# Optimization experiments

Hardware: AMD Instinct MI355X
Metric: run time of the kernel (lower is better)

The kernel has to match this reference:

```python
import jax, jax.numpy as jnp
import numpy as np


def _selective_scan(u, delta, A, Bm, Cm, Dskip, delta_bias):
    # u, delta: (B, K*D, L); A: (K*D, N); Bm, Cm: (B, K, N, L); Dskip, delta_bias: (K*D,)
    Bsz, KD, L = u.shape
    K = Bm.shape[1]
    D = KD // K
    N = A.shape[1]
    dt = jax.nn.softplus(delta + delta_bias[None, :, None])          # (B,KD,L)
    u4 = u.reshape(Bsz, K, D, L)
    dt4 = dt.reshape(Bsz, K, D, L)
    A4 = A.reshape(K, D, N)
    # discretization: dA = exp(dt*A), dBu = dt * B * u
    dA = jnp.exp(dt4[..., None] * A4[None, :, :, None, :])            # (B,K,D,L,N)
    Bt = jnp.transpose(Bm, (0, 1, 3, 2))                               # (B,K,L,N)
    dBu = dt4[..., None] * u4[..., None] * Bt[:, :, None, :, :]        # (B,K,D,L,N)
    dA_l = jnp.moveaxis(dA, 3, 0)                                      # (L,B,K,D,N)
    dBu_l = jnp.moveaxis(dBu, 3, 0)

    def step(h, ab):
        a, b = ab
        h = a * h + b
        return h, h

    h0 = jnp.zeros(dA_l.shape[1:], dA.dtype)
    _, hs = jax.lax.scan(step, h0, (dA_l, dBu_l))                      # (L,B,K,D,N)
    C_l = jnp.moveaxis(Cm, 3, 0)                                       # (L,B,K,N)
    y = jnp.einsum('lbkdn,lbkn->lbkd', hs, C_l)                        # (L,B,K,D)
    y = jnp.moveaxis(y, 0, 3).reshape(Bsz, KD, L)
    return y + u * Dskip[None, :, None]


def setup_inputs() -> dict:
    key = jax.random.key(0)
    ks = jax.random.split(key, 8)
    B, H, W, C = 2, 64, 64, 96
    Di, N, K = 192, 16, 4
    R = 6  # ceil(96/16)
    x = jax.random.normal(ks[0], (B, H, W, C), jnp.float32)
    in_proj_w = jax.random.normal(ks[1], (2 * Di, C), jnp.float32) * (C ** -0.5)
    conv_w = jax.random.normal(ks[2], (Di, 1, 3, 3), jnp.float32) * 0.2
    conv_b = jax.random.normal(ks[3], (Di,), jnp.float32) * 0.02
    x_proj_weight = jax.random.normal(ks[4], (K, R + 2 * N, Di), jnp.float32) * (Di ** -0.5)
    dt_projs_weight = jax.random.uniform(ks[5], (K, Di, R), jnp.float32, -(R ** -0.5), R ** -0.5)
    dt = jnp.exp(jax.random.uniform(ks[6], (K, Di), jnp.float32) * (np.log(0.1) - np.log(0.001)) + np.log(0.001))
    dt = jnp.clip(dt, 1e-4)
    dt_projs_bias = dt + jnp.log(-jnp.expm1(-dt))                      # inverse softplus
    A_logs = jnp.log(jnp.tile(jnp.arange(1, N + 1, dtype=jnp.float32), (K * Di, 1)))
    Ds = jnp.ones((K * Di,), jnp.float32)
    out_norm_w = jnp.ones((Di,), jnp.float32)
    out_norm_b = jnp.zeros((Di,), jnp.float32)
    out_proj_w = jax.random.normal(ks[7], (C, Di), jnp.float32) * (Di ** -0.5)
    return dict(x=x, in_proj_w=in_proj_w, conv_w=conv_w, conv_b=conv_b,
                x_proj_weight=x_proj_weight, dt_projs_weight=dt_projs_weight,
                dt_projs_bias=dt_projs_bias, A_logs=A_logs, Ds=Ds,
                out_norm_w=out_norm_w, out_norm_b=out_norm_b, out_proj_w=out_proj_w)


def reference(x, in_proj_w, conv_w, conv_b, x_proj_weight, dt_projs_weight,
              dt_projs_bias, A_logs, Ds, out_norm_w, out_norm_b, out_proj_w):
    Bsz, H, W, C = x.shape
    Di = conv_w.shape[0]
    K = x_proj_weight.shape[0]
    R = dt_projs_weight.shape[2]
    N = A_logs.shape[1]
    L = H * W
    # in_proj (bias=False) and split into x, z
    xz = x @ in_proj_w.T                                               # (B,H,W,2*Di)
    xi, z = jnp.split(xz, 2, axis=-1)
    # depthwise conv2d + SiLU (channel-first)
    xc = jnp.transpose(xi, (0, 3, 1, 2))                               # (B,Di,H,W)
    xc = jax.lax.conv_general_dilated(xc, conv_w, (1, 1), 'SAME',
                                      feature_group_count=Di) + conv_b[None, :, None, None]
    xc = jax.nn.silu(xc)
    # cross-scan: 4 directions (row-major, col-major, and their reverses)
    x0 = xc.reshape(Bsz, Di, L)
    x1 = jnp.transpose(xc, (0, 1, 3, 2)).reshape(Bsz, Di, L)
    xs = jnp.stack([x0, x1, x0[..., ::-1], x1[..., ::-1]], axis=1)      # (B,K,Di,L)
    # per-direction projections
    x_dbl = jnp.einsum('bkdl,kcd->bkcl', xs, x_proj_weight)            # (B,K,R+2N,L)
    dts, Bs, Cs = jnp.split(x_dbl, [R, R + N], axis=2)
    dts = jnp.einsum('bkrl,kdr->bkdl', dts, dt_projs_weight)           # (B,K,Di,L)
    A = -jnp.exp(A_logs)                                               # (K*Di,N)
    ys = _selective_scan(xs.reshape(Bsz, K * Di, L), dts.reshape(Bsz, K * Di, L),
                         A, Bs, Cs, Ds, dt_projs_bias.reshape(-1))
    ys = ys.reshape(Bsz, K, Di, L)
    # cross-merge
    y = ys[:, 0] + ys[:, 2, :, ::-1]
    yt = ys[:, 1] + ys[:, 3, :, ::-1]                                  # col-major ordering
    y = y + jnp.transpose(yt.reshape(Bsz, Di, W, H), (0, 1, 3, 2)).reshape(Bsz, Di, L)
    y = jnp.transpose(y.reshape(Bsz, Di, H, W), (0, 2, 3, 1))          # (B,H,W,Di)
    # out_norm: LayerNorm over channel
    mu = jnp.mean(y, axis=-1, keepdims=True)
    var = jnp.mean((y - mu) ** 2, axis=-1, keepdims=True)
    y = (y - mu) * jax.lax.rsqrt(var + 1e-5) * out_norm_w + out_norm_b
    # gate and out_proj (bias=False)
    y = y * jax.nn.silu(z)
    return y @ out_proj_w.T
```

## Files before the change

### kernel.cpp

```cpp
#include <hip/hip_runtime.h>
#include <hip/hip_fp16.h>
#include <math.h>


static constexpr int Bsz = 2;
static constexpr int Lc  = 4096;
static constexpr int Cc  = 96;
static constexpr int Dd  = 192;
static constexpr int Kk  = 4;
static constexpr int NC  = 32;

__device__ __forceinline__ float bu(unsigned short v) {
    return __uint_as_float((unsigned int)v << 16);
}
__device__ __forceinline__ unsigned short f2b(float f) {
    unsigned int u = __float_as_uint(f);
    return (unsigned short)((u + 0x7fffu + ((u >> 16) & 1u)) >> 16);
}

template<int CTRL>
__device__ __forceinline__ float dppadd(float x) {
    return x + __int_as_float(__builtin_amdgcn_update_dpp(
        0, __float_as_int(x), CTRL, 0xf, 0xf, true));
}
__device__ __forceinline__ float red16(float x) {
    x = dppadd<0xB1>(x);
    x = dppadd<0x4E>(x);
    x = dppadd<0x124>(x);
    x = dppadd<0x128>(x);
    return x;
}

__global__ __launch_bounds__(256) void k0_detect(const unsigned short* __restrict__ x,
                                                 int* __restrict__ flag)
{
    __shared__ int s[256];
    int cnt = 0;
    for (int i = threadIdx.x; i < 4096; i += 256) {
        int e = (x[i] >> 7) & 0xFF;
        cnt += (e >= 118 && e <= 131) ? 1 : 0;
    }
    s[threadIdx.x] = cnt;
    __syncthreads();
    for (int st = 128; st > 0; st >>= 1) {
        if (threadIdx.x < st) s[threadIdx.x] += s[threadIdx.x + st];
        __syncthreads();
    }
    if (threadIdx.x == 0) flag[0] = (s[0] >= 3072) ? 1 : 0;
}

struct Cv {
    const void* src[11];
    int off[11];
    int n[11];
};
__global__ __launch_bounds__(256) void k0b_convert(Cv cv, const int* __restrict__ flag,
                                                   float* __restrict__ dstbase)
{
    int bf = flag[0];
    int t = blockIdx.y;
    int i = blockIdx.x * 256 + threadIdx.x;
    if (i >= cv.n[t]) return;
    float v;
    if (bf) v = bu(((const unsigned short*)cv.src[t])[i]);
    else    v = ((const float*)cv.src[t])[i];
    dstbase[cv.off[t] + i] = v;
}

__global__ __launch_bounds__(256) void k3w_prep(const float* __restrict__ xpwf,
                                                float* __restrict__ Wg)
{
    int idx = blockIdx.x * 256 + threadIdx.x;
    if (idx >= 4 * 192 * 40) return;
    int cp = idx % 40;
    int d  = (idx / 40) % 192;
    int k  = idx / 7680;
    Wg[idx] = (cp < 38) ? xpwf[(size_t)(k * 38 + cp) * 192 + d] : 0.f;
}

__global__ __launch_bounds__(256) void k1_inproj(const void* __restrict__ xraw,
                                                 const int* __restrict__ flag,
                                                 const float* __restrict__ wf,
                                                 float* __restrict__ xi, __half* __restrict__ zs)
{
    __shared__ float xT[32 * 97];
    __shared__ float wT[96 * 97];
    const int bf = flag[0];
    int tile = blockIdx.x >> 2, jq = blockIdx.x & 3;
    int b = tile >> 7;
    int l0 = (tile & 127) << 5;
    int j0 = jq * 96;
    for (int e = threadIdx.x; e < 32 * 96; e += 256) {
        int i = e / 96, c = e % 96;
        size_t idx = (size_t)(b * Lc + l0 + i) * Cc + c;
        xT[i * 97 + c] = bf ? bu(((const unsigned short*)xraw)[idx])
                            : ((const float*)xraw)[idx];
    }
    for (int e = threadIdx.x; e < 96 * 96; e += 256) {
        int j = e / 96, c = e % 96;
        wT[j * 97 + c] = wf[(size_t)(j0 + j) * Cc + c];
    }
    __syncthreads();
    int jj = threadIdx.x & 31, ll = threadIdx.x >> 5;
    float acc[4][3];
#pragma unroll
    for (int i = 0; i < 4; i++)
#pragma unroll
        for (int m = 0; m < 3; m++) acc[i][m] = 0.f;
    for (int c = 0; c < 96; ++c) {
        float xv[4], wv[3];
#pragma unroll
        for (int i = 0; i < 4; i++) xv[i] = xT[(ll * 4 + i) * 97 + c];
#pragma unroll
        for (int m = 0; m < 3; m++) wv[m] = wT[(jj + 32 * m) * 97 + c];
#pragma unroll
        for (int i = 0; i < 4; i++)
#pragma unroll
            for (int m = 0; m < 3; m++) acc[i][m] += xv[i] * wv[m];
    }
#pragma unroll
    for (int i = 0; i < 4; i++) {
        int l = l0 + ll * 4 + i;
#pragma unroll
        for (int m = 0; m < 3; m++) {
            int j = j0 + jj + 32 * m;
            float v = acc[i][m];
            if (j < Dd) xi[(size_t)(b * Lc + l) * Dd + j] = v;
            else        zs[(size_t)(b * Lc + l) * Dd + (j - Dd)] = __float2half(v / (1.f + __expf(-v)));
        }
    }
}

__global__ __launch_bounds__(256) void k2a_transpose(const float* __restrict__ xi,
                                                     float* __restrict__ xiT)
{
    __shared__ float t[64 * 65];
    int bid = blockIdx.x;
    int lq = bid & 63, dq = (bid >> 6) % 3, b = bid / 192;
    int l0 = lq * 64, d0 = dq * 64;
    for (int e = threadIdx.x; e < 4096; e += 256) {
        int i = e >> 6, j = e & 63;
        t[i * 65 + j] = xi[(size_t)(b * Lc + l0 + i) * Dd + d0 + j];
    }
    __syncthreads();
    for (int e = threadIdx.x; e < 4096; e += 256) {
        int j = e >> 6, i = e & 63;
        xiT[(size_t)(b * Dd + d0 + j) * Lc + l0 + i] = t[i * 65 + j];
    }
}

__global__ __launch_bounds__(256) void k2b_conv(const float* __restrict__ xiT,
                                                const float* __restrict__ cwf,
                                                const float* __restrict__ cbf,
                                                float* __restrict__ xc,
                                                float* __restrict__ uT)
{
    __shared__ float inl[34 * 66];
    __shared__ float outl[32 * 65];
    int bid = blockIdx.x;
    int half = bid & 1;
    int d = (bid >> 1) % Dd;
    int b = bid / (2 * Dd);
    int h0 = half * 32;
    const float* src = xiT + (size_t)(b * Dd + d) * Lc;
    for (int r = threadIdx.x; r < 34; r += 256) {
        inl[r * 66 + 0] = 0.f;
        inl[r * 66 + 65] = 0.f;
    }
    for (int e = threadIdx.x; e < 34 * 64; e += 256) {
        int row = e >> 6, w = e & 63;
        int h = h0 - 1 + row;
        inl[row * 66 + 1 + w] = (h >= 0 && h < 64) ? src[h * 64 + w] : 0.f;
    }
    __syncthreads();
    float wgt[9];
#pragma unroll
    for (int t = 0; t < 9; t++) wgt[t] = cwf[d * 9 + t];
    float bias = cbf[d];
    int hs = threadIdx.x >> 6, w = threadIdx.x & 63;
    float* dstrow = xc + (size_t)(b * Dd + d) * Lc;
#pragma unroll
    for (int it = 0; it < 8; ++it) {
        int hh = it * 4 + hs;
        float acc = bias;
#pragma unroll
        for (int dy = 0; dy < 3; ++dy) {
            const float* rp = &inl[(hh + dy) * 66 + w];
#pragma unroll
            for (int dx = 0; dx < 3; ++dx)
                acc += rp[dx] * wgt[dy * 3 + dx];
        }
        float s = acc / (1.f + __expf(-acc));
        dstrow[(h0 + hh) * 64 + w] = s;
        outl[hh * 65 + w] = s;
    }
    __syncthreads();
    float* udst = uT + (size_t)(b * Dd + d) * Lc;
    for (int e = threadIdx.x; e < 2048; e += 256) {
        int w2 = e >> 5, hh2 = e & 31;
        udst[w2 * 64 + h0 + hh2] = outl[hh2 * 65 + w2];
    }
}

__global__ __launch_bounds__(256) void k3_proj(const float* __restrict__ xc,
                                               const float* __restrict__ uT,
                                               const float* __restrict__ Wg,
                                               const float* __restrict__ dtwf,
                                               const float* __restrict__ dtbf,
                                               __half* __restrict__ dtH,
                                               float* __restrict__ BsT, float* __restrict__ CsT)
{
    __shared__ float rawdt[6][64];
    int bid = blockIdx.x;
    int pt = bid & 63, k = (bid >> 6) & 3, b = bid >> 8;
    int s0 = pt * 64;
    int pi = threadIdx.x & 63;
    int q  = __builtin_amdgcn_readfirstlane(threadIdx.x >> 6);

    const float* xb = ((k & 1) ? uT : xc) + (size_t)b * Dd * Lc + s0 + pi;
    const float* wk = Wg + (size_t)k * 192 * 40 + q * 10;

    float acc[10];
#pragma unroll
    for (int j = 0; j < 10; ++j) acc[j] = 0.f;

    for (int d = 0; d < 192; ++d) {
        float xv = xb[(size_t)d * Lc];
        const float* wrow = wk + d * 40;
#pragma unroll
        for (int j = 0; j < 10; ++j) acc[j] += wrow[j] * xv;
    }

    if (q == 0) {
#pragma unroll
        for (int j = 0; j < 6; ++j) rawdt[j][pi] = acc[j];
    }
    size_t bk16 = (size_t)(b * Kk + k) * 16;
#pragma unroll
    for (int j = 0; j < 10; ++j) {
        int cp = q * 10 + j;
        if (cp >= 6 && cp < 22)
            BsT[(bk16 + (cp - 6)) * Lc + s0 + pi] = acc[j];
        else if (cp >= 22 && cp < 38)
            CsT[(bk16 + (cp - 22)) * Lc + s0 + pi] = acc[j];
    }
    __syncthreads();

    float raws[6];
#pragma unroll
    for (int r = 0; r < 6; ++r) raws[r] = rawdt[r][pi];
    const float* dtw = dtwf + (size_t)(k * 192 + q * 48) * 6;
    const float* dtb = dtbf + k * 192 + q * 48;
    __half* dto = dtH + ((size_t)(b * Kk + k) * Dd + q * 48) * Lc + s0 + pi;
    for (int dd = 0; dd < 48; ++dd) {
        float s = dtb[dd];
#pragma unroll
        for (int r = 0; r < 6; ++r) s += raws[r] * dtw[dd * 6 + r];
        float sp = fmaxf(s, 0.f) + log1pf(__expf(-fabsf(s)));
        dto[(size_t)dd * Lc] = __float2half(sp);
    }
}

template<int REV, int PASS3>
__device__ __forceinline__ void scan_run(const float* __restrict__ ubase,
                                         const __half* __restrict__ dbase,
                                         const float* __restrict__ Bbase,
                                         const float* __restrict__ Cbase,
                                         float* uL, float* bL, float* cL, __half* dL,
                                         int dl, int n, int c,
                                         float An, float Dsv,
                                         float* __restrict__ P, float* __restrict__ S,
                                         size_t pidx, __half* __restrict__ yrow)
{
    const int t0 = c * 128;
    const int tg = REV ? (Lc - 128 - t0) : t0;

    {
        float4 ru0 = *reinterpret_cast<const float4*>(ubase + tg + n * 4);
        float4 ru1 = *reinterpret_cast<const float4*>(ubase + tg + 64 + n * 4);
        float4 rb0 = *reinterpret_cast<const float4*>(Bbase + tg + n * 4);
        float4 rb1 = *reinterpret_cast<const float4*>(Bbase + tg + 64 + n * 4);
        uint4  rd  = *reinterpret_cast<const uint4*>(dbase + tg + n * 8);
        *reinterpret_cast<float4*>(uL + dl * 132 + n * 4) = ru0;
        *reinterpret_cast<float4*>(uL + dl * 132 + 64 + n * 4) = ru1;
        *reinterpret_cast<float4*>(bL + dl * 132 + n * 4) = rb0;
        *reinterpret_cast<float4*>(bL + dl * 132 + 64 + n * 4) = rb1;
        *reinterpret_cast<uint4*>(dL + dl * 136 + n * 8) = rd;
        if (PASS3) {
            float4 rc0 = *reinterpret_cast<const float4*>(Cbase + tg + n * 4);
            float4 rc1 = *reinterpret_cast<const float4*>(Cbase + tg + 64 + n * 4);
            *reinterpret_cast<float4*>(cL + dl * 132 + n * 4) = rc0;
            *reinterpret_cast<float4*>(cL + dl * 132 + 64 + n * 4) = rc1;
        }
    }
    __syncthreads();

    float h = PASS3 ? P[pidx] : 0.f;
    float sdt = 0.f, ystash = 0.f;

#pragma unroll 4
    for (int qi = 0; qi < 32; ++qi) {
        const int col4 = REV ? (124 - qi * 4) : (qi * 4);
        float4 uq = *reinterpret_cast<const float4*>(uL + dl * 132 + col4);
        float4 bq = *reinterpret_cast<const float4*>(bL + n * 132 + col4);
        float4 cq{};
        if (PASS3) cq = *reinterpret_cast<const float4*>(cL + n * 132 + col4);
        uint2 dq = *reinterpret_cast<const uint2*>(dL + dl * 136 + col4);
        const __half2* dh2 = reinterpret_cast<const __half2*>(&dq);
#pragma unroll
        for (int j = 0; j < 4; ++j) {
            const int e = REV ? (3 - j) : j;
            float dtv = (e & 1) ? __high2float(dh2[e >> 1]) : __low2float(dh2[e >> 1]);
            float uv = reinterpret_cast<const float*>(&uq)[e];
            float bv = reinterpret_cast<const float*>(&bq)[e];
            float a = __expf(dtv * An);
            if (!PASS3) sdt += dtv;
            h = a * h + (dtv * uv) * bv;
            if (PASS3) {
                float cv = reinterpret_cast<const float*>(&cq)[e];
                float yv = red16(h * cv);
                const int i15 = (qi & 3) * 4 + j;
                if (i15 == n) ystash = yv + uv * Dsv;
                if (i15 == 15) {
                    int tb = t0 + (qi >> 2) * 16 + n;
                    int aw = REV ? (Lc - 1 - tb) : tb;
                    yrow[aw] = __float2half(ystash);
                }
            }
        }
    }

    if (!PASS3) {
        P[pidx] = __expf(An * sdt);
        S[pidx] = h;
    }
}

template<int PASS3>
__global__ __launch_bounds__(256) void kscan(const __half* __restrict__ dtH,
                                             const float* __restrict__ xc,
                                             const float* __restrict__ uT,
                                             const float* __restrict__ BsT,
                                             const float* __restrict__ CsT,
                                             const float* __restrict__ alogf,
                                             const float* __restrict__ dsf,
                                             float* __restrict__ P,
                                             float* __restrict__ S,
                                             __half* __restrict__ ysH)
{
    __shared__ float uL[16 * 132];
    __shared__ float bL[16 * 132];
    __shared__ float cL[PASS3 ? 16 * 132 : 4];
    __shared__ __half dL[16 * 136];

    int c  = blockIdx.x & 31;
    int t1 = blockIdx.x >> 5;
    int dg = t1 % 12;
    int kk = (t1 / 12) & 3;
    int b  = t1 / 48;
    int n  = threadIdx.x & 15, dl = threadIdx.x >> 4;
    int d  = dg * 16 + dl;

    const float* ubz = ((kk & 1) ? uT : xc) + (size_t)b * Dd * Lc;
    const float*  ubase = ubz + (size_t)d * Lc;
    const __half* dbase = dtH + ((size_t)((b * Kk + kk) * Dd + d)) * Lc;
    const float*  Bbase = BsT + ((size_t)((b * Kk + kk) * 16 + dl)) * Lc;
    const float*  Cbase = CsT + ((size_t)((b * Kk + kk) * 16 + dl)) * Lc;

    float An  = -__expf(alogf[(kk * Dd + d) * 16 + n]);
    float Dsv = PASS3 ? dsf[kk * Dd + d] : 0.f;
    size_t pidx = (((size_t)(b * Kk + kk) * Dd + d) * NC + c) * 16 + n;
    __half* yrow = PASS3 ? ysH + ((size_t)(kk * Bsz + b) * Dd + d) * Lc : nullptr;

    if (kk >= 2)
        scan_run<1, PASS3>(ubase, dbase, Bbase, Cbase, uL, bL, cL, dL,
                           dl, n, c, An, Dsv, P, S, pidx, yrow);
    else
        scan_run<0, PASS3>(ubase, dbase, Bbase, Cbase, uL, bL, cL, dL,
                           dl, n, c, An, Dsv, P, S, pidx, yrow);
}

__global__ __launch_bounds__(256) void k6_pass2(float* __restrict__ P, const float* __restrict__ S)
{
    int g = blockIdx.x * 256 + threadIdx.x;
    int n = g & 15;
    int chain = g >> 4;
    size_t base = (size_t)chain * NC * 16 + n;
    float h = 0.f;
    for (int c = 0; c < NC; ++c) {
        size_t id = base + (size_t)c * 16;
        float p = P[id], s = S[id];
        P[id] = h;
        h = p * h + s;
    }
}

__global__ __launch_bounds__(256) void k8t(const __half* __restrict__ ysH,
                                           __half* __restrict__ ysT)
{
    __shared__ float t[64 * 65];
    int bid = blockIdx.x;
    int d = bid % Dd, b = bid / Dd;
    const __half* y1 = ysH + ((size_t)(1 * Bsz + b) * Dd + d) * Lc;
    const __half* y3 = ysH + ((size_t)(3 * Bsz + b) * Dd + d) * Lc;
    __half* dst = ysT + ((size_t)b * Dd + d) * Lc;
    for (int e = threadIdx.x; e < 4096; e += 256)
        t[(e >> 6) * 65 + (e & 63)] = __half2float(y1[e]) + __half2float(y3[e]);
    __syncthreads();
    for (int e = threadIdx.x; e < 4096; e += 256)
        dst[e] = __float2half(t[(e & 63) * 65 + (e >> 6)]);
}

__global__ __launch_bounds__(256) void k8_norm(const __half* __restrict__ ysH,
                                               const __half* __restrict__ ysT,
                                               const __half* __restrict__ zsH,
                                               const float* __restrict__ nwf,
                                               const float* __restrict__ nbf,
                                               __half* __restrict__ gH)
{
    __shared__ float yt[192 * 33];
    __shared__ float ps1[8 * 32], ps2[8 * 32];
    __shared__ float mu[32], rs[32];
    int bid = blockIdx.x;
    int pt = bid & 127, b = bid >> 7;
    int p0 = pt * 32;
    for (int e = threadIdx.x; e < 192 * 32; e += 256) {
        int d = e >> 5, p = e & 31;
        size_t r0 = ((size_t)(0 * Bsz + b) * Dd + d) * Lc + p0 + p;
        size_t r2 = ((size_t)(2 * Bsz + b) * Dd + d) * Lc + p0 + p;
        size_t rt = ((size_t)b * Dd + d) * Lc + p0 + p;
        yt[d * 33 + p] = __half2float(ysH[r0]) + __half2float(ysH[r2]) + __half2float(ysT[rt]);
    }
    __syncthreads();
    {
        int p = threadIdx.x & 31, q = threadIdx.x >> 5;
        float s1 = 0.f, s2 = 0.f;
        for (int dd = 0; dd < 24; ++dd) {
            float v = yt[(q * 24 + dd) * 33 + p];
            s1 += v; s2 += v * v;
        }
        ps1[q * 32 + p] = s1; ps2[q * 32 + p] = s2;
    }
    __syncthreads();
    if (threadIdx.x < 32) {
        int p = threadIdx.x;
        float s1 = 0.f, s2 = 0.f;
        for (int q = 0; q < 8; ++q) { s1 += ps1[q * 32 + p]; s2 += ps2[q * 32 + p]; }
        float m = s1 * (1.f / 192.f);
        float var = s2 * (1.f / 192.f) - m * m;
        mu[p] = m; rs[p] = rsqrtf(var + 1e-5f);
    }
    __syncthreads();
    for (int i = threadIdx.x; i < 32 * 192; i += 256) {
        int p = i / 192, d = i - p * 192;
        float v = (yt[d * 33 + p] - mu[p]) * rs[p] * nwf[d] + nbf[d];
        size_t addr = ((size_t)b * Lc + p0 + p) * Dd + d;
        float zv = __half2float(zsH[addr]);
        gH[addr] = __float2half(v * zv);
    }
}

__global__ __launch_bounds__(256) void k10_outproj(const __half* __restrict__ gH,
                                                   const float* __restrict__ wof,
                                                   const int* __restrict__ flag,
                                                   void* __restrict__ outv)
{
    __shared__ float wT[192 * 100];
    const int bf = flag[0];
    for (int e = threadIdx.x; e < 96 * 192; e += 256) {
        int cI = e / 192, dI = e - cI * 192;
        wT[dI * 100 + cI] = wof[e];
    }
    __syncthreads();
    int r0 = blockIdx.x * 32;
    int r = threadIdx.x >> 3, cg = threadIdx.x & 7;
    const __half* grow = gH + (size_t)(r0 + r) * Dd;
    float acc[12];
#pragma unroll
    for (int i = 0; i < 12; ++i) acc[i] = 0.f;
    for (int d0 = 0; d0 < 192; d0 += 8) {
        __half2 g2[4];
        *reinterpret_cast<uint4*>(g2) = *reinterpret_cast<const uint4*>(grow + d0);
#pragma unroll
        for (int j = 0; j < 8; ++j) {
            float gf = (j & 1) ? __high2float(g2[j >> 1]) : __low2float(g2[j >> 1]);
            const float* wrow = &wT[(d0 + j) * 100 + cg * 12];
            float4 w0 = *reinterpret_cast<const float4*>(wrow);
            float4 w1 = *reinterpret_cast<const float4*>(wrow + 4);
            float4 w2 = *reinterpret_cast<const float4*>(wrow + 8);
            acc[0] += gf * w0.x; acc[1] += gf * w0.y; acc[2]  += gf * w0.z; acc[3]  += gf * w0.w;
            acc[4] += gf * w1.x; acc[5] += gf * w1.y; acc[6]  += gf * w1.z; acc[7]  += gf * w1.w;
            acc[8] += gf * w2.x; acc[9] += gf * w2.y; acc[10] += gf * w2.z; acc[11] += gf * w2.w;
        }
    }
    size_t obase = (size_t)(r0 + r) * Cc + cg * 12;
    if (bf) {
        unsigned short* o = (unsigned short*)outv;
#pragma unroll
        for (int cc = 0; cc < 12; ++cc) o[obase + cc] = f2b(acc[cc]);
    } else {
        float* o = (float*)outv;
#pragma unroll
        for (int cc = 0; cc < 12; ++cc) o[obase + cc] = acc[cc];
    }
}

extern "C" void kernel_launch(void* const* d_in, const int* in_sizes, int n_in,
                              void* d_out, int out_size, void* d_ws, size_t ws_size,
                              hipStream_t stream)
{
    (void)out_size; (void)ws_size;
    float* ws = (float*)d_ws;
    int* flag = (int*)ws;

    int off[12]; int tot = 64;
    off[0] = 0;
    for (int i = 1; i < 12; ++i) {
        off[i] = tot;
        int n = (i < n_in) ? in_sizes[i] : 0;
        tot += (n + 63) & ~63;
    }
    float* winf = ws + off[1];
    float* cwf  = ws + off[2];
    float* cbf  = ws + off[3];
    float* xpwf = ws + off[4];
    float* dtwf = ws + off[5];
    float* dtbf = ws + off[6];
    float* alogf= ws + off[7];
    float* dsf  = ws + off[8];
    float* nwf  = ws + off[9];
    float* nbf  = ws + off[10];
    float* wof  = ws + off[11];

    const size_t BASE = 131072;
    __half* dtH = (__half*)(ws + BASE);
    float*  xc  = ws + BASE + 3145728;
    float*  uT  = ws + BASE + 4718592;
    float*  BsT = ws + BASE + 6291456;
    float*  CsT = ws + BASE + 6815744;
    float*  P   = ws + BASE + 7340032;
    float*  S   = ws + BASE + 8126464;
    __half* zsH = (__half*)(ws + BASE + 8912896);
    float*  xi  = ws + BASE + 9699328;
    float*  xiT = ws + BASE + 9699328 + 1572864;
    __half* ysH = (__half*)(ws + BASE + 9699328);
    __half* ysT = (__half*)P;
    __half* gH  = (__half*)S;
    float*  Wg  = ws + BASE + 12845056;

    Cv cv;
    for (int i = 0; i < 11; ++i) {
        int t = i + 1;
        cv.src[i] = (t < n_in) ? d_in[t] : d_in[0];
        cv.off[i] = off[t];
        cv.n[i]   = (t < n_in) ? in_sizes[t] : 0;
    }

    k0_detect   <<<dim3(1),    dim3(256), 0, stream>>>((const unsigned short*)d_in[0], flag);
    k0b_convert <<<dim3(144, 11), dim3(256), 0, stream>>>(cv, flag, ws);
    k3w_prep    <<<dim3(120),  dim3(256), 0, stream>>>(xpwf, Wg);
    k1_inproj   <<<dim3(1024), dim3(256), 0, stream>>>(d_in[0], flag, winf, xi, zsH);
    k2a_transpose<<<dim3(384), dim3(256), 0, stream>>>(xi, xiT);
    k2b_conv    <<<dim3(768),  dim3(256), 0, stream>>>(xiT, cwf, cbf, xc, uT);
    k3_proj     <<<dim3(512),  dim3(256), 0, stream>>>(xc, uT, Wg, dtwf, dtbf, dtH, BsT, CsT);
    kscan<0>    <<<dim3(3072), dim3(256), 0, stream>>>(dtH, xc, uT, BsT, CsT, alogf, dsf, P, S, ysH);
    k6_pass2    <<<dim3(96),   dim3(256), 0, stream>>>(P, S);
    kscan<1>    <<<dim3(3072), dim3(256), 0, stream>>>(dtH, xc, uT, BsT, CsT, alogf, dsf, P, S, ysH);
    k8t         <<<dim3(384),  dim3(256), 0, stream>>>(ysH, ysT);
    k8_norm     <<<dim3(256),  dim3(256), 0, stream>>>(ysH, ysT, zsH, nwf, nbf, gH);
    k10_outproj <<<dim3(256),  dim3(256), 0, stream>>>(gH, wof, flag, d_out);
}
```

Before: 200.8 us.

## Fuse transpose into in-proj, fold weight prep and D-skip into other kernels

The in-projection now writes its x half directly in channel-major layout and z as a transposed half-precision gate, which removes the separate transpose kernel. The x_proj weight repack is merged into the input conversion kernel as an extra grid row. The D-skip term leaves the scan kernel; the norm kernel adds it once, using the summed D across the four directions applied to the conv output. The pass-2 kernel now runs 64-thread blocks with an unrolled loop. Together these cut two launches and one full intermediate round trip, at the cost of weights being read from global memory inside the in-proj inner loop instead of from LDS.

```diff
diff --git a/kernel.cpp b/kernel.cpp
--- a/kernel.cpp
+++ b/kernel.cpp
@@ -50,9 +50,9 @@
 }
 
 struct Cv {
-    const void* src[11];
-    int off[11];
-    int n[11];
+    const void* src[12];
+    int off[12];
+    int n[12];
 };
 __global__ __launch_bounds__(256) void k0b_convert(Cv cv, const int* __restrict__ flag,
                                                    float* __restrict__ dstbase)
@@ -61,91 +61,72 @@
     int t = blockIdx.y;
     int i = blockIdx.x * 256 + threadIdx.x;
     if (i >= cv.n[t]) return;
+    if (t == 11) {
+        int cp = i % 40;
+        int d  = (i / 40) % 192;
+        int k  = i / 7680;
+        float v = 0.f;
+        if (cp < 38) {
+            size_t si = (size_t)(k * 38 + cp) * 192 + d;
+            v = bf ? bu(((const unsigned short*)cv.src[11])[si])
+                   : ((const float*)cv.src[11])[si];
+        }
+        dstbase[cv.off[11] + i] = v;
+        return;
+    }
     float v;
     if (bf) v = bu(((const unsigned short*)cv.src[t])[i]);
     else    v = ((const float*)cv.src[t])[i];
     dstbase[cv.off[t] + i] = v;
 }
 
-__global__ __launch_bounds__(256) void k3w_prep(const float* __restrict__ xpwf,
-                                                float* __restrict__ Wg)
-{
-    int idx = blockIdx.x * 256 + threadIdx.x;
-    if (idx >= 4 * 192 * 40) return;
-    int cp = idx % 40;
-    int d  = (idx / 40) % 192;
-    int k  = idx / 7680;
-    Wg[idx] = (cp < 38) ? xpwf[(size_t)(k * 38 + cp) * 192 + d] : 0.f;
-}
-
 __global__ __launch_bounds__(256) void k1_inproj(const void* __restrict__ xraw,
                                                  const int* __restrict__ flag,
                                                  const float* __restrict__ wf,
-                                                 float* __restrict__ xi, __half* __restrict__ zs)
-{
-    __shared__ float xT[32 * 97];
-    __shared__ float wT[96 * 97];
+                                                 float* __restrict__ xiT, __half* __restrict__ zT)
+{
+    __shared__ float xT[64 * 97];
     const int bf = flag[0];
-    int tile = blockIdx.x >> 2, jq = blockIdx.x & 3;
-    int b = tile >> 7;
-    int l0 = (tile & 127) << 5;
-    int j0 = jq * 96;
-    for (int e = threadIdx.x; e < 32 * 96; e += 256) {
+    int lt = blockIdx.x & 127;
+    int jq = blockIdx.x >> 7;
+    int row0 = lt * 64;
+    for (int e = threadIdx.x; e < 64 * 96; e += 256) {
         int i = e / 96, c = e % 96;
-        size_t idx = (size_t)(b * Lc + l0 + i) * Cc + c;
+        size_t idx = (size_t)(row0 + i) * Cc + c;
         xT[i * 97 + c] = bf ? bu(((const unsigned short*)xraw)[idx])
                             : ((const float*)xraw)[idx];
     }
-    for (int e = threadIdx.x; e < 96 * 96; e += 256) {
-        int j = e / 96, c = e % 96;
-        wT[j * 97 + c] = wf[(size_t)(j0 + j) * Cc + c];
-    }
-    __syncthreads();
-    int jj = threadIdx.x & 31, ll = threadIdx.x >> 5;
-    float acc[4][3];
-#pragma unroll
-    for (int i = 0; i < 4; i++)
-#pragma unroll
-        for (int m = 0; m < 3; m++) acc[i][m] = 0.f;
-    for (int c = 0; c < 96; ++c) {
-        float xv[4], wv[3];
-#pragma unroll
-        for (int i = 0; i < 4; i++) xv[i] = xT[(ll * 4 + i) * 97 + c];
-#pragma unroll
-        for (int m = 0; m < 3; m++) wv[m] = wT[(jj + 32 * m) * 97 + c];
-#pragma unroll
-        for (int i = 0; i < 4; i++)
-#pragma unroll
-            for (int m = 0; m < 3; m++) acc[i][m] += xv[i] * wv[m];
-    }
-#pragma unroll
-    for (int i = 0; i < 4; i++) {
-        int l = l0 + ll * 4 + i;
-#pragma unroll
-        for (int m = 0; m < 3; m++) {
-            int j = j0 + jj + 32 * m;
-            float v = acc[i][m];
-            if (j < Dd) xi[(size_t)(b * Lc + l) * Dd + j] = v;
-            else        zs[(size_t)(b * Lc + l) * Dd + (j - Dd)] = __float2half(v / (1.f + __expf(-v)));
-        }
-    }
-}
-
-__global__ __launch_bounds__(256) void k2a_transpose(const float* __restrict__ xi,
-                                                     float* __restrict__ xiT)
-{
-    __shared__ float t[64 * 65];
-    int bid = blockIdx.x;
-    int lq = bid & 63, dq = (bid >> 6) % 3, b = bid / 192;
-    int l0 = lq * 64, d0 = dq * 64;
-    for (int e = threadIdx.x; e < 4096; e += 256) {
-        int i = e >> 6, j = e & 63;
-        t[i * 65 + j] = xi[(size_t)(b * Lc + l0 + i) * Dd + d0 + j];
-    }
-    __syncthreads();
-    for (int e = threadIdx.x; e < 4096; e += 256) {
-        int j = e >> 6, i = e & 63;
-        xiT[(size_t)(b * Dd + d0 + j) * Lc + l0 + i] = t[i * 65 + j];
+    __syncthreads();
+    int pi = threadIdx.x & 63;
+    int q  = __builtin_amdgcn_readfirstlane(threadIdx.x >> 6);
+    int j0 = jq * 96 + q * 24;
+    float acc[24];
+#pragma unroll
+    for (int j = 0; j < 24; ++j) acc[j] = 0.f;
+    for (int c4 = 0; c4 < 24; ++c4) {
+        float xv0 = xT[pi * 97 + c4 * 4 + 0];
+        float xv1 = xT[pi * 97 + c4 * 4 + 1];
+        float xv2 = xT[pi * 97 + c4 * 4 + 2];
+        float xv3 = xT[pi * 97 + c4 * 4 + 3];
+#pragma unroll
+        for (int j = 0; j < 24; ++j) {
+            float4 w4 = *reinterpret_cast<const float4*>(&wf[(size_t)(j0 + j) * 96 + c4 * 4]);
+            acc[j] += w4.x * xv0 + w4.y * xv1 + w4.z * xv2 + w4.w * xv3;
+        }
+    }
+    int b = row0 >> 12;
+    int l = (row0 & 4095) + pi;
+    if (jq < 2) {
+#pragma unroll
+        for (int j = 0; j < 24; ++j)
+            xiT[((size_t)b * Dd + j0 + j) * Lc + l] = acc[j];
+    } else {
+#pragma unroll
+        for (int j = 0; j < 24; ++j) {
+            float v = acc[j];
+            zT[((size_t)b * Dd + (j0 + j - 192)) * Lc + l] =
+                __float2half(v / (1.f + __expf(-v)));
+        }
     }
 }
 
@@ -268,7 +249,7 @@
                                          const float* __restrict__ Cbase,
                                          float* uL, float* bL, float* cL, __half* dL,
                                          int dl, int n, int c,
-                                         float An, float Dsv,
+                                         float An,
                                          float* __restrict__ P, float* __restrict__ S,
                                          size_t pidx, __half* __restrict__ yrow)
 {
@@ -320,7 +301,7 @@
                 float cv = reinterpret_cast<const float*>(&cq)[e];
                 float yv = red16(h * cv);
                 const int i15 = (qi & 3) * 4 + j;
-                if (i15 == n) ystash = yv + uv * Dsv;
+                if (i15 == n) ystash = yv;
                 if (i15 == 15) {
                     int tb = t0 + (qi >> 2) * 16 + n;
                     int aw = REV ? (Lc - 1 - tb) : tb;
@@ -343,7 +324,6 @@
                                              const float* __restrict__ BsT,
                                              const float* __restrict__ CsT,
                                              const float* __restrict__ alogf,
-                                             const float* __restrict__ dsf,
                                              float* __restrict__ P,
                                              float* __restrict__ S,
                                              __half* __restrict__ ysH)
@@ -368,25 +348,25 @@
     const float*  Cbase = CsT + ((size_t)((b * Kk + kk) * 16 + dl)) * Lc;
 
     float An  = -__expf(alogf[(kk * Dd + d) * 16 + n]);
-    float Dsv = PASS3 ? dsf[kk * Dd + d] : 0.f;
     size_t pidx = (((size_t)(b * Kk + kk) * Dd + d) * NC + c) * 16 + n;
     __half* yrow = PASS3 ? ysH + ((size_t)(kk * Bsz + b) * Dd + d) * Lc : nullptr;
 
     if (kk >= 2)
         scan_run<1, PASS3>(ubase, dbase, Bbase, Cbase, uL, bL, cL, dL,
-                           dl, n, c, An, Dsv, P, S, pidx, yrow);
+                           dl, n, c, An, P, S, pidx, yrow);
     else
         scan_run<0, PASS3>(ubase, dbase, Bbase, Cbase, uL, bL, cL, dL,
-                           dl, n, c, An, Dsv, P, S, pidx, yrow);
-}
-
-__global__ __launch_bounds__(256) void k6_pass2(float* __restrict__ P, const float* __restrict__ S)
-{
-    int g = blockIdx.x * 256 + threadIdx.x;
+                           dl, n, c, An, P, S, pidx, yrow);
+}
+
+__global__ __launch_bounds__(64) void k6_pass2(float* __restrict__ P, const float* __restrict__ S)
+{
+    int g = blockIdx.x * 64 + threadIdx.x;
     int n = g & 15;
     int chain = g >> 4;
     size_t base = (size_t)chain * NC * 16 + n;
     float h = 0.f;
+#pragma unroll
     for (int c = 0; c < NC; ++c) {
         size_t id = base + (size_t)c * 16;
         float p = P[id], s = S[id];
@@ -413,7 +393,9 @@
 
 __global__ __launch_bounds__(256) void k8_norm(const __half* __restrict__ ysH,
                                                const __half* __restrict__ ysT,
-                                               const __half* __restrict__ zsH,
+                                               const __half* __restrict__ zT,
+                                               const float* __restrict__ xc,
+                                               const float* __restrict__ dsf,
                                                const float* __restrict__ nwf,
                                                const float* __restrict__ nbf,
                                                __half* __restrict__ gH)
@@ -429,7 +411,10 @@
         size_t r0 = ((size_t)(0 * Bsz + b) * Dd + d) * Lc + p0 + p;
         size_t r2 = ((size_t)(2 * Bsz + b) * Dd + d) * Lc + p0 + p;
         size_t rt = ((size_t)b * Dd + d) * Lc + p0 + p;
-        yt[d * 33 + p] = __half2float(ysH[r0]) + __half2float(ysH[r2]) + __half2float(ysT[rt]);
+        float ds4 = dsf[d] + dsf[192 + d] + dsf[384 + d] + dsf[576 + d];
+        yt[d * 33 + p] = __half2float(ysH[r0]) + __half2float(ysH[r2])
+                       + __half2float(ysT[rt])
+                       + xc[((size_t)b * Dd + d) * Lc + p0 + p] * ds4;
     }
     __syncthreads();
     {
@@ -451,12 +436,16 @@
         mu[p] = m; rs[p] = rsqrtf(var + 1e-5f);
     }
     __syncthreads();
+    for (int e = threadIdx.x; e < 192 * 32; e += 256) {
+        int d = e >> 5, p = e & 31;
+        float v = (yt[d * 33 + p] - mu[p]) * rs[p] * nwf[d] + nbf[d];
+        float zv = __half2float(zT[((size_t)b * Dd + d) * Lc + p0 + p]);
+        yt[d * 33 + p] = v * zv;
+    }
+    __syncthreads();
     for (int i = threadIdx.x; i < 32 * 192; i += 256) {
         int p = i / 192, d = i - p * 192;
-        float v = (yt[d * 33 + p] - mu[p]) * rs[p] * nwf[d] + nbf[d];
-        size_t addr = ((size_t)b * Lc + p0 + p) * Dd + d;
-        float zv = __half2float(zsH[addr]);
-        gH[addr] = __float2half(v * zv);
+        gH[((size_t)b * Lc + p0 + p) * Dd + d] = __float2half(yt[d * 33 + p]);
     }
 }
 
@@ -523,7 +512,6 @@
     float* winf = ws + off[1];
     float* cwf  = ws + off[2];
     float* cbf  = ws + off[3];
-    float* xpwf = ws + off[4];
     float* dtwf = ws + off[5];
     float* dtbf = ws + off[6];
     float* alogf= ws + off[7];
@@ -540,9 +528,8 @@
     float*  CsT = ws + BASE + 6815744;
     float*  P   = ws + BASE + 7340032;
     float*  S   = ws + BASE + 8126464;
-    __half* zsH = (__half*)(ws + BASE + 8912896);
-    float*  xi  = ws + BASE + 9699328;
-    float*  xiT = ws + BASE + 9699328 + 1572864;
+    __half* zT  = (__half*)(ws + BASE + 8912896);
+    float*  xiT = ws + BASE + 9699328;
     __half* ysH = (__half*)(ws + BASE + 9699328);
     __half* ysT = (__half*)P;
     __half* gH  = (__half*)S;
@@ -555,18 +542,21 @@
         cv.off[i] = off[t];
         cv.n[i]   = (t < n_in) ? in_sizes[t] : 0;
     }
+    Cv cv2;
+    for (int i = 0; i < 11; ++i) { cv2.src[i] = cv.src[i]; cv2.off[i] = cv.off[i]; cv2.n[i] = cv.n[i]; }
+    cv2.src[11] = (4 < n_in) ? d_in[4] : d_in[0];
+    cv2.off[11] = (int)(BASE + 12845056);
+    cv2.n[11]   = 4 * 192 * 40;
 
     k0_detect   <<<dim3(1),    dim3(256), 0, stream>>>((const unsigned short*)d_in[0], flag);
-    k0b_convert <<<dim3(144, 11), dim3(256), 0, stream>>>(cv, flag, ws);
-    k3w_prep    <<<dim3(120),  dim3(256), 0, stream>>>(xpwf, Wg);
-    k1_inproj   <<<dim3(1024), dim3(256), 0, stream>>>(d_in[0], flag, winf, xi, zsH);
-    k2a_transpose<<<dim3(384), dim3(256), 0, stream>>>(xi, xiT);
+    k0b_convert <<<dim3(144, 12), dim3(256), 0, stream>>>(cv2, flag, ws);
+    k1_inproj   <<<dim3(512),  dim3(256), 0, stream>>>(d_in[0], flag, winf, xiT, zT);
     k2b_conv    <<<dim3(768),  dim3(256), 0, stream>>>(xiT, cwf, cbf, xc, uT);
     k3_proj     <<<dim3(512),  dim3(256), 0, stream>>>(xc, uT, Wg, dtwf, dtbf, dtH, BsT, CsT);
-    kscan<0>    <<<dim3(3072), dim3(256), 0, stream>>>(dtH, xc, uT, BsT, CsT, alogf, dsf, P, S, ysH);
-    k6_pass2    <<<dim3(96),   dim3(256), 0, stream>>>(P, S);
-    kscan<1>    <<<dim3(3072), dim3(256), 0, stream>>>(dtH, xc, uT, BsT, CsT, alogf, dsf, P, S, ysH);
+    kscan<0>    <<<dim3(3072), dim3(256), 0, stream>>>(dtH, xc, uT, BsT, CsT, alogf, P, S, ysH);
+    k6_pass2    <<<dim3(384),  dim3(64),  0, stream>>>(P, S);
+    kscan<1>    <<<dim3(3072), dim3(256), 0, stream>>>(dtH, xc, uT, BsT, CsT, alogf, P, S, ysH);
     k8t         <<<dim3(384),  dim3(256), 0, stream>>>(ysH, ysT);
-    k8_norm     <<<dim3(256),  dim3(256), 0, stream>>>(ysH, ysT, zsH, nwf, nbf, gH);
+    k8_norm     <<<dim3(256),  dim3(256), 0, stream>>>(ysH, ysT, zT, xc, dsf, nwf, nbf, gH);
     k10_outproj <<<dim3(256),  dim3(256), 0, stream>>>(gH, wof, flag, d_out);
 }
```

Result: faster. 196.8 us (-2.0%).
